# Kernel tuning notes

Measured on AMD Instinct MI355X. Metric: run time of the kernel, lower is better.

Reference implementation:

```python
import jax, jax.numpy as jnp
import numpy as np

B, S, IN = 64, 2048, 256          # batch, num_steps, input_size
MS, H, HD = 8, 8, 64              # mem_slots, num_heads, head_size
M = H * HD                        # mem_size = 512
KS = HD                           # key_size defaults to head_size
NG = 2 * M                        # num_gates (gate_style='unit')
TOPK = 3
EPS = 1e-5


def layernorm(x, g, b):
    mu = jnp.mean(x, axis=-1, keepdims=True)
    var = jnp.var(x, axis=-1, keepdims=True)
    return (x - mu) / jnp.sqrt(var + EPS) * g + b


def setup_inputs() -> dict:
    key = jax.random.key(0)
    ks = jax.random.split(key, 16)
    def w(k, shape, scale=0.02):
        return jax.random.normal(k, shape, dtype=jnp.float32) * scale
    return {
        "inputs": jax.random.normal(ks[0], (B, S, IN), dtype=jnp.float32),
        "memory": jax.random.normal(ks[1], (B, MS, M), dtype=jnp.float32),
        "Wq": w(ks[2], (M, H * KS)), "bq": jnp.zeros((H * KS,), jnp.float32),
        "Wk": w(ks[3], (M, H * KS)), "bk": jnp.zeros((H * KS,), jnp.float32),
        "Wv": w(ks[4], (M, H * HD)), "bv": jnp.zeros((H * HD,), jnp.float32),
        "Wmlp": w(ks[5], (M, M)), "bmlp": jnp.zeros((M,), jnp.float32),  # shared across both mlp layers ([Linear]*L)
        "g1": jnp.ones((M,), jnp.float32), "b1": jnp.zeros((M,), jnp.float32),
        "g2": jnp.ones((M,), jnp.float32), "b2": jnp.zeros((M,), jnp.float32),
        "Wi": w(ks[6], (IN, M)), "bi": jnp.zeros((M,), jnp.float32),  # input_projector
        "rw": jax.random.normal(ks[7], (M,), dtype=jnp.float32),       # RepeatLinear.w
        "Wr": w(ks[8], (M, NG)), "br": jnp.zeros((NG,), jnp.float32),  # RepeatLinear.linear
        "Wg": w(ks[9], (MS, M, NG)),                                   # GroupLinearLayer (no bias)
        "forget_bias": jnp.array(1.0, jnp.float32),
        "input_bias": jnp.array(0.0, jnp.float32),
    }


def reference(inputs, memory, Wq, bq, Wk, bk, Wv, bv, Wmlp, bmlp,
              g1, b1, g2, b2, Wi, bi, rw, Wr, br, Wg,
              forget_bias, input_bias):
    # input_projector (treat_input_as_matrix=True path)
    x = inputs @ Wi + bi                                   # [B,S,M]

    # --- multihead attention over memory (num_blocks=1) ---
    q = (memory @ Wq + bq).reshape(B, MS, H, KS).transpose(0, 2, 1, 3)   # [B,H,MS,KS]
    k = (x @ Wk + bk).reshape(B, S, H, KS).transpose(0, 2, 1, 3)         # [B,H,S,KS]
    v = (x @ Wv + bv).reshape(B, S, H, HD).transpose(0, 2, 1, 3)         # [B,H,S,HD]
    scores = jax.nn.softmax(jnp.einsum('bhmd,bhsd->bhms', q, k), axis=-1)  # no 1/sqrt(d) scale, per source
    # top-k mask over key/step axis, scatter of top-k indices -> multiplicative 0/1 mask
    _, idx = jax.lax.top_k(scores, TOPK)                   # [B,H,MS,TOPK]
    mask = jnp.sum(jax.nn.one_hot(idx, S, dtype=scores.dtype), axis=-2)  # [B,H,MS,S]
    scores = scores * mask
    att = jnp.einsum('bhms,bhsd->bhmd', scores, v)         # [B,H,MS,HD]
    att = att.transpose(0, 2, 1, 3).reshape(B, MS, M)      # [B,MS,M]

    mem1 = layernorm(memory + att, g1, b1)
    mlp = jax.nn.relu(mem1 @ Wmlp + bmlp)                  # attention_mlp layer (weights shared)
    mlp = jax.nn.relu(mlp @ Wmlp + bmlp)
    next_mem = layernorm(mem1 + mlp, g2, b2)

    # --- gates (computed from pre-attention memory, per forward_step) ---
    gate_in = jax.nn.relu(rw * x).mean(axis=1) @ Wr + br   # RepeatLinear -> [B,NG]
    gate_mem = jnp.einsum('bsd,sdo->bso', jnp.tanh(memory), Wg)  # GroupLinear -> [B,MS,NG]
    gates = gate_mem + gate_in[:, None, :]
    input_gate, forget_gate = jnp.split(gates, 2, axis=2)  # each [B,MS,M]
    input_gate = jax.nn.sigmoid(input_gate + input_bias)
    forget_gate = jax.nn.sigmoid(forget_gate + forget_bias)

    next_mem = input_gate * jnp.tanh(next_mem) + forget_gate * memory
    return next_mem.reshape(B, MS * M)
```

## Files before the change

### kernel.cpp

```cpp
#include <hip/hip_runtime.h>
#include <hip/hip_bf16.h>
#include <math.h>

#define BB 64
#define SS 2048
#define IN_ 256
#define MSLOT 8
#define HH 8
#define HD_ 64
#define MM 512
#define NG_ 1024

typedef __attribute__((ext_vector_type(8))) short short8;
typedef __attribute__((ext_vector_type(8))) unsigned short ushort8;
typedef __attribute__((ext_vector_type(4))) unsigned short ushort4v;
typedef __attribute__((ext_vector_type(4))) float f32x4;
typedef __attribute__((ext_vector_type(16))) float f32x16;
typedef unsigned long long u64;
typedef unsigned int u32;

__device__ __forceinline__ unsigned short f2bf(float f) {
    unsigned int u = __builtin_bit_cast(unsigned int, f);
    u += 0x7fff + ((u >> 16) & 1);
    return (unsigned short)(u >> 16);
}

__device__ __forceinline__ u64 score_key(float v, int idx) {
    u32 x = __float_as_uint(v);
    u32 fk = (x & 0x80000000u) ? ~x : (x | 0x80000000u);
    return ((u64)fk << 32) | (u32)(~(u32)idx);
}
__device__ __forceinline__ float key_val(u64 k) {
    u32 fk = (u32)(k >> 32);
    u32 x = (fk & 0x80000000u) ? (fk & 0x7FFFFFFFu) : ~fk;
    return __uint_as_float(x);
}
__device__ __forceinline__ int key_idx(u64 k) { return (int)(~(u32)k); }

__device__ __forceinline__ void merge3(u64& a0, u64& a1, u64& a2, u64 b0, u64 b1, u64 b2) {
    bool t0 = a0 >= b0;
    u64 m0 = t0 ? a0 : b0;
    u64 a0x = t0 ? a1 : a0, a1x = t0 ? a2 : a1;
    u64 b0x = t0 ? b0 : b1, b1x = t0 ? b1 : b2;
    bool t1 = a0x >= b0x;
    u64 m1 = t1 ? a0x : b0x;
    u64 a0y = t1 ? a1x : a0x;
    u64 b0y = t1 ? b0x : b1x;
    bool t2 = a0y >= b0y;
    u64 m2 = t2 ? a0y : b0y;
    a0 = m0; a1 = m1; a2 = m2;
}

__device__ __forceinline__ void merge3_shfl(u64& k0, u64& k1, u64& k2, int off) {
    u64 b0 = __shfl_xor(k0, off);
    u64 b1 = __shfl_xor(k1, off);
    u64 b2 = __shfl_xor(k2, off);
    merge3(k0, k1, k2, b0, b1, b2);
}

__device__ __forceinline__ float block_sum256(float v, float* red) {
    int t = threadIdx.x;
    red[t] = v; __syncthreads();
    for (int s = 128; s > 0; s >>= 1) {
        if (t < s) red[t] += red[t + s];
        __syncthreads();
    }
    float r = red[0];
    __syncthreads();
    return r;
}

__device__ __forceinline__ void stage_tile_f32cvt(unsigned short* lds,
                                                  const float* __restrict__ src,
                                                  int t) {
#pragma unroll
    for (int it = 0; it < 8; ++it) {
        int c = t + it * 256;
        int r = c >> 5, ch = c & 31;
        const float* p = src + (size_t)r * 256 + ch * 8;
        float4 f0 = *(const float4*)p;
        float4 f1 = *(const float4*)(p + 4);
        ushort8 v;
        v[0] = f2bf(f0.x); v[1] = f2bf(f0.y); v[2] = f2bf(f0.z); v[3] = f2bf(f0.w);
        v[4] = f2bf(f1.x); v[5] = f2bf(f1.y); v[6] = f2bf(f1.z); v[7] = f2bf(f1.w);
        int sch = ch ^ (r & 15);
        *(ushort8*)(lds + r * 256 + sch * 8) = v;
    }
}

__device__ __forceinline__ short8 frag_ld(const unsigned short* lds, int row, int chunk) {
    int sch = chunk ^ (row & 15);
    return *(const short8*)(lds + row * 256 + sch * 8);
}

__device__ __forceinline__ short8 frag_ld512(const unsigned short* lds, int row, int chunk) {
    int sch = chunk ^ (row & 7);
    return *(const short8*)(lds + row * 512 + sch * 8);
}

__global__ __launch_bounds__(256) void k_fuse_w(const float* __restrict__ Wi,
                                                const float* __restrict__ Wk,
                                                const float* __restrict__ Wv,
                                                const float* __restrict__ bi,
                                                const float* __restrict__ bv,
                                                float* __restrict__ WikT,
                                                float* __restrict__ Wiv,
                                                float* __restrict__ bvf) {
    int blk = blockIdx.x;
    int which = blk >> 9;
    int o = blk & 511;
    const float* W = which ? Wv : Wk;

    __shared__ float col[512];
    __shared__ float red[256];
    int t = threadIdx.x;
    col[t]       = W[t * 512 + o];
    col[t + 256] = W[(t + 256) * 512 + o];
    __syncthreads();

    const float* wi_row = Wi + t * 512;
    float acc = 0.f;
    for (int j = 0; j < 512; ++j) acc += wi_row[j] * col[j];
    if (which) Wiv[t * 512 + o] = acc;
    else       WikT[o * 256 + t] = acc;

    if (which) {
        float p = bi[t] * col[t] + bi[t + 256] * col[t + 256];
        float s = block_sum256(p, red);
        if (t == 0) bvf[o] = s + bv[o];
    }
}

__global__ __launch_bounds__(256) void k_q(const float* __restrict__ memory,
                                           const float* __restrict__ Wq,
                                           const float* __restrict__ bq,
                                           float* __restrict__ q) {
    int bms = blockIdx.x;
    __shared__ float row[512];
    int t = threadIdx.x;
    row[t]       = memory[bms * 512 + t];
    row[t + 256] = memory[bms * 512 + t + 256];
    __syncthreads();
    for (int oo = 0; oo < 2; ++oo) {
        int o = oo * 256 + t;
        float acc = bq[o];
        for (int j = 0; j < 512; ++j) acc += row[j] * Wq[j * 512 + o];
        q[bms * 512 + o] = acc;
    }
}

__global__ __launch_bounds__(256) void k_p(const float* __restrict__ q,
                                           const float* __restrict__ WikT,
                                           unsigned short* __restrict__ Pb) {
    int blk = blockIdx.x;
    int b = blk >> 6, hm = blk & 63;
    int h = hm >> 3, ms = hm & 7;
    int t = threadIdx.x;
    __shared__ float qv[64];
    if (t < 64) qv[t] = q[(b * 8 + ms) * 512 + h * 64 + t];
    __syncthreads();
    float acc = 0.f;
    for (int d = 0; d < 64; ++d) acc += qv[d] * WikT[(h * 64 + d) * 256 + t];
    Pb[blk * 256 + t] = f2bf(acc);
}

__global__ __launch_bounds__(256) void k_prep(const float* __restrict__ Wi,
                                              unsigned short* __restrict__ WiTf,
                                              const float* __restrict__ mem,
                                              unsigned short* __restrict__ tm,
                                              const float* __restrict__ Wmlp,
                                              unsigned short* __restrict__ WmlpTb) {
    int blk = blockIdx.x;
    int t = threadIdx.x;
    if (blk < 512) {
        int idx = blk * 256 + t;
        int e = idx & 7, l = (idx >> 3) & 63, ks = (idx >> 9) & 15, dtg = idx >> 13;
        int d = dtg * 32 + (l & 31);
        int k = ks * 16 + (l >> 5) * 8 + e;
        WiTf[idx] = f2bf(Wi[k * 512 + d]);
    } else if (blk < 768) {
        int i = ((blk - 512) * 256 + t) * 4;
        float4 v = *(const float4*)(mem + i);
        ushort4v o;
        o[0] = f2bf(tanhf(v.x)); o[1] = f2bf(tanhf(v.y));
        o[2] = f2bf(tanhf(v.z)); o[3] = f2bf(tanhf(v.w));
        *(ushort4v*)(tm + i) = o;
    } else {
        int o = blk - 768;
#pragma unroll
        for (int kk = 0; kk < 2; ++kk) {
            int k = kk * 256 + t;
            WmlpTb[o * 512 + k] = f2bf(Wmlp[k * 512 + o]);
        }
    }
}

__global__ __launch_bounds__(256) void k_big(const float* __restrict__ inputs,
                                             const unsigned short* __restrict__ Pb,
                                             const unsigned short* __restrict__ WiTf,
                                             const float* __restrict__ bi,
                                             const float* __restrict__ rw,
                                             uint4* __restrict__ statA,
                                             uint4* __restrict__ statB,
                                             float* __restrict__ giaccp) {
    __shared__ unsigned short Il[64 * 256];
    int t = threadIdx.x;
    int hw = blockIdx.x;
    int L = (hw & 7) * 256 + (hw >> 3);
    int b = L >> 5, stile = L & 31;
    int l = t & 63, w = t >> 6;
    int kg = l >> 4, r16 = l & 15;
    int l31 = l & 31, hi = l >> 5;

    stage_tile_f32cvt(Il, inputs + ((size_t)b * SS + stile * 64) * IN_, t);
    __syncthreads();

    f32x4 acc[4];
#pragma unroll
    for (int nt = 0; nt < 4; ++nt) acc[nt] = (f32x4){0.f, 0.f, 0.f, 0.f};
    {
        const unsigned short* pbase = Pb + ((size_t)(b * 64 + w * 16 + r16)) * 256;
#pragma unroll
        for (int kk = 0; kk < 8; ++kk) {
            short8 a = *(const short8*)(pbase + kk * 32 + kg * 8);
#pragma unroll
            for (int nt = 0; nt < 4; ++nt) {
                short8 bfr = frag_ld(Il, nt * 16 + r16, kk * 4 + kg);
                acc[nt] = __builtin_amdgcn_mfma_f32_16x16x32_bf16(a, bfr, acc[nt], 0, 0, 0);
            }
        }
    }

    int sbase = stile * 64;
#pragma unroll
    for (int j = 0; j < 4; ++j) {
        u64 k0 = 0, k1 = 0, k2 = 0;
#pragma unroll
        for (int nt = 0; nt < 4; ++nt) {
            u64 key = score_key(acc[nt][j], sbase + nt * 16 + r16);
            bool g0 = key > k0, g1 = key > k1, g2 = key > k2;
            k2 = g1 ? k1 : (g2 ? key : k2);
            k1 = g0 ? k0 : (g1 ? key : k1);
            k0 = g0 ? key : k0;
        }
        merge3_shfl(k0, k1, k2, 1);
        merge3_shfl(k0, k1, k2, 2);
        merge3_shfl(k0, k1, k2, 4);
        merge3_shfl(k0, k1, k2, 8);

        float m = key_val(k0);
        float se = 0.f;
#pragma unroll
        for (int nt = 0; nt < 4; ++nt) se += expf(acc[nt][j] - m);
#pragma unroll
        for (int off = 1; off <= 8; off <<= 1) se += __shfl_xor(se, off);

        if (r16 == 0) {
            int row = w * 16 + kg * 4 + j;
            int grow = (b * 64 + row) * 32 + stile;
            statA[grow] = make_uint4(__float_as_uint(se), (u32)(k0 >> 32), (u32)k0, (u32)(k1 >> 32));
            statB[grow] = make_uint4((u32)k1, (u32)(k2 >> 32), (u32)k2, 0u);
        }
    }

#pragma unroll 1
    for (int i = 0; i < 4; ++i) {
        int dtg = w * 4 + i;
        int d = dtg * 32 + l31;
        float bid = bi[d], rwd = rw[d];
        f32x16 g0 = {0.f,0.f,0.f,0.f,0.f,0.f,0.f,0.f,0.f,0.f,0.f,0.f,0.f,0.f,0.f,0.f};
        f32x16 g1 = {0.f,0.f,0.f,0.f,0.f,0.f,0.f,0.f,0.f,0.f,0.f,0.f,0.f,0.f,0.f,0.f};
#pragma unroll
        for (int ksh = 0; ksh < 2; ++ksh) {
            short8 wf[8];
#pragma unroll
            for (int ks8 = 0; ks8 < 8; ++ks8)
                wf[ks8] = *(const short8*)(WiTf + ((size_t)((dtg * 16 + ksh * 8 + ks8) * 64) + l) * 8);
#pragma unroll
            for (int ks8 = 0; ks8 < 8; ++ks8) {
                int ch = (ksh * 8 + ks8) * 2 + hi;
                short8 a0 = frag_ld(Il, l31, ch);
                g0 = __builtin_amdgcn_mfma_f32_32x32x16_bf16(a0, wf[ks8], g0, 0, 0, 0);
                short8 a1 = frag_ld(Il, 32 + l31, ch);
                g1 = __builtin_amdgcn_mfma_f32_32x32x16_bf16(a1, wf[ks8], g1, 0, 0, 0);
            }
        }
        float rs = 0.f;
#pragma unroll
        for (int jj = 0; jj < 16; ++jj) {
            rs += fmaxf(rwd * (g0[jj] + bid), 0.f);
            rs += fmaxf(rwd * (g1[jj] + bid), 0.f);
        }
        rs += __shfl_xor(rs, 32);
        if (hi == 0)
            giaccp[((size_t)stile * 64 + b) * 512 + d] = rs;
    }
}

__global__ __launch_bounds__(256) void k_combine(const uint4* __restrict__ statA,
                                                 const uint4* __restrict__ statB,
                                                 float* __restrict__ topk_p,
                                                 int* __restrict__ topk_idx) {
    int t = threadIdx.x;
    int row = blockIdx.x * 4 + (t >> 6);
    int l = t & 63;

    float s_c = 0.f, m_c = 0.f;
    u64 k0 = 0, k1 = 0, k2 = 0;
    if (l < 32) {
        uint4 A = statA[row * 32 + l];
        uint4 Bv = statB[row * 32 + l];
        s_c = __uint_as_float(A.x);
        k0 = ((u64)A.y << 32) | A.z;
        k1 = ((u64)A.w << 32) | Bv.x;
        k2 = ((u64)Bv.y << 32) | Bv.z;
        m_c = key_val(k0);
    }
    merge3_shfl(k0, k1, k2, 1);
    merge3_shfl(k0, k1, k2, 2);
    merge3_shfl(k0, k1, k2, 4);
    merge3_shfl(k0, k1, k2, 8);
    merge3_shfl(k0, k1, k2, 16);

    float M = key_val(k0);
    float S = (l < 32) ? s_c * expf(m_c - M) : 0.f;
#pragma unroll
    for (int off = 1; off <= 16; off <<= 1) S += __shfl_xor(S, off);

    if (l == 0) {
        u64 ks[3] = {k0, k1, k2};
#pragma unroll
        for (int r = 0; r < 3; ++r) {
            topk_p[row * 3 + r] = expf(key_val(ks[r]) - M) / S;
            topk_idx[row * 3 + r] = key_idx(ks[r]);
        }
    }
}

__global__ __launch_bounds__(256) void k_att2(const float* __restrict__ inputs,
                                              const float* __restrict__ Wiv,
                                              const float* __restrict__ bvf,
                                              const float* __restrict__ topk_p,
                                              const int* __restrict__ topk_idx,
                                              const float* __restrict__ memory,
                                              const float* __restrict__ g1,
                                              const float* __restrict__ b1,
                                              float* __restrict__ mem1) {
    int bms = blockIdx.x;
    int b = bms >> 3, ms = bms & 7;
    int t = threadIdx.x;
    __shared__ float w[8 * 256];
    __shared__ float ps[8];
    __shared__ float red[256];

#pragma unroll
    for (int h = 0; h < 8; ++h) {
        int row = (b * 64 + h * 8 + ms) * 3;
        float acc = 0.f, psum = 0.f;
#pragma unroll
        for (int j = 0; j < 3; ++j) {
            int sj = topk_idx[row + j];
            float pj = topk_p[row + j];
            acc += pj * inputs[((size_t)b * SS + sj) * IN_ + t];
            psum += pj;
        }
        w[h * 256 + t] = acc;
        if (t == 0) ps[h] = psum;
    }
    __syncthreads();

    float a_val[2];
#pragma unroll
    for (int oo = 0; oo < 2; ++oo) {
        int o = oo * 256 + t;
        int h = o >> 6;
        float acc = ps[h] * bvf[o];
        const float* wh = w + h * 256;
#pragma unroll 8
        for (int i = 0; i < 256; ++i) acc += wh[i] * Wiv[i * 512 + o];
        a_val[oo] = acc;
    }

    float m0 = memory[bms * 512 + t], m1 = memory[bms * 512 + t + 256];
    float x0 = m0 + a_val[0], x1 = m1 + a_val[1];
    float mu = block_sum256(x0 + x1, red) * (1.f / 512.f);
    float d0 = x0 - mu, d1 = x1 - mu;
    float var = block_sum256(d0 * d0 + d1 * d1, red) * (1.f / 512.f);
    float rstd = rsqrtf(var + 1e-5f);
    mem1[bms * 512 + t]       = d0 * rstd * g1[t] + b1[t];
    mem1[bms * 512 + t + 256] = d1 * rstd * g1[t + 256] + b1[t + 256];
}

__global__ __launch_bounds__(256) void k_gatein2(const float* __restrict__ giaccp,
                                                 const float* __restrict__ Wr,
                                                 const float* __restrict__ br,
                                                 float* __restrict__ gate_in) {
    int b = blockIdx.x >> 2, ot = blockIdx.x & 3;
    int t = threadIdx.x;
    int o = ot * 256 + t;
    __shared__ float gm[512];
    float s0 = 0.f, s1 = 0.f;
    for (int st = 0; st < 32; ++st) {
        s0 += giaccp[((size_t)st * 64 + b) * 512 + t];
        s1 += giaccp[((size_t)st * 64 + b) * 512 + t + 256];
    }
    gm[t]       = s0 * (1.0f / 2048.0f);
    gm[t + 256] = s1 * (1.0f / 2048.0f);
    __syncthreads();
    float acc = br[o];
#pragma unroll 8
    for (int d = 0; d < 512; ++d) acc += gm[d] * Wr[d * 1024 + o];
    gate_in[b * 1024 + o] = acc;
}

__global__ __launch_bounds__(256) void k_gates_mfma(const unsigned short* __restrict__ tmem_b,
                                                    const float* __restrict__ Wg,
                                                    const float* __restrict__ gate_in,
                                                    const float* __restrict__ fb,
                                                    const float* __restrict__ ib,
                                                    float* __restrict__ sg) {
    int ms = blockIdx.x >> 5;
    int otile = blockIdx.x & 31;
    int t = threadIdx.x;
    int l = t & 63, w = t >> 6;
    int kg = l >> 4, r16 = l & 15;
    __shared__ unsigned short Al[64 * 128];
    __shared__ unsigned short Bl[32 * 136];
    f32x4 acc[2];
#pragma unroll
    for (int nt = 0; nt < 2; ++nt) acc[nt] = (f32x4){0.f, 0.f, 0.f, 0.f};

    int o_l = t & 31;
    for (int kc = 0; kc < 4; ++kc) {
        __syncthreads();
#pragma unroll
        for (int it = 0; it < 4; ++it) {
            int c = t + it * 256;
            int r = c >> 4, ch = c & 15;
            ushort8 v = *(const ushort8*)(tmem_b + (size_t)(r * 8 + ms) * 512 + kc * 128 + ch * 8);
            int sch = ch ^ (r & 7);
            *(ushort8*)(Al + r * 128 + sch * 8) = v;
        }
#pragma unroll
        for (int i = 0; i < 16; ++i) {
            int k_l = (t >> 5) + 8 * i;
            float v = Wg[((size_t)ms * 512 + kc * 128 + k_l) * 1024 + otile * 32 + o_l];
            Bl[o_l * 136 + k_l] = f2bf(v);
        }
        __syncthreads();
#pragma unroll
        for (int kk = 0; kk < 4; ++kk) {
            int ch = kk * 4 + kg;
            short8 a = *(const short8*)(Al + (w * 16 + r16) * 128 + ((ch ^ (r16 & 7)) * 8));
#pragma unroll
            for (int nt = 0; nt < 2; ++nt) {
                short8 bfr = *(const short8*)(Bl + (nt * 16 + r16) * 136 + ch * 8);
                acc[nt] = __builtin_amdgcn_mfma_f32_16x16x32_bf16(a, bfr, acc[nt], 0, 0, 0);
            }
        }
    }
    float ibv = ib[0], fbv = fb[0];
#pragma unroll
    for (int nt = 0; nt < 2; ++nt) {
        int o = otile * 32 + nt * 16 + r16;
        float bias = (o < 512) ? ibv : fbv;
#pragma unroll
        for (int j = 0; j < 4; ++j) {
            int b = w * 16 + kg * 4 + j;
            float g = acc[nt][j] + gate_in[b * 1024 + o] + bias;
            sg[(size_t)(b * 8 + ms) * 1024 + o] = 1.f / (1.f + expf(-g));
        }
    }
}

__global__ __launch_bounds__(256) void k_mlp_mfma(const float* __restrict__ mem1,
                                                  const unsigned short* __restrict__ WmlpTb,
                                                  const float* __restrict__ bmlp,
                                                  const float* __restrict__ g2,
                                                  const float* __restrict__ b2,
                                                  const float* __restrict__ sg,
                                                  const float* __restrict__ memory,
                                                  float* __restrict__ out) {
    __shared__ unsigned short At[16 * 512];
    __shared__ unsigned short Bt[16 * 512];
    __shared__ float redS[64], redQ[64], muL[16], rsL[16];
    int blk = blockIdx.x;
    int rowbase = blk * 16;
    int t = threadIdx.x;
    int l = t & 63, w = t >> 6;
    int kg = l >> 4, r16 = l & 15;

#pragma unroll
    for (int it = 0; it < 4; ++it) {
        int c = t + it * 256;
        int r = c >> 6, ch = c & 63;
        const float* p = mem1 + (size_t)(rowbase + r) * 512 + ch * 8;
        float4 f0 = *(const float4*)p;
        float4 f1 = *(const float4*)(p + 4);
        ushort8 v;
        v[0] = f2bf(f0.x); v[1] = f2bf(f0.y); v[2] = f2bf(f0.z); v[3] = f2bf(f0.w);
        v[4] = f2bf(f1.x); v[5] = f2bf(f1.y); v[6] = f2bf(f1.z); v[7] = f2bf(f1.w);
        int sch = ch ^ (r & 7);
        *(ushort8*)(At + r * 512 + sch * 8) = v;
    }
    __syncthreads();

    f32x4 acc[8];
#pragma unroll
    for (int f = 0; f < 8; ++f) acc[f] = (f32x4){0.f, 0.f, 0.f, 0.f};
    for (int kk2 = 0; kk2 < 16; ++kk2) {
        short8 a = frag_ld512(At, r16, kk2 * 4 + kg);
#pragma unroll
        for (int f = 0; f < 8; ++f) {
            short8 bfr = *(const short8*)(WmlpTb + (size_t)(w * 128 + f * 16 + r16) * 512 + kk2 * 32 + kg * 8);
            acc[f] = __builtin_amdgcn_mfma_f32_16x16x32_bf16(a, bfr, acc[f], 0, 0, 0);
        }
    }
#pragma unroll
    for (int f = 0; f < 8; ++f) {
        int o = w * 128 + f * 16 + r16;
        float bm = bmlp[o];
        int ch = o >> 3, oe = o & 7;
#pragma unroll
        for (int j = 0; j < 4; ++j) {
            int row = kg * 4 + j;
            float v = fmaxf(acc[f][j] + bm, 0.f);
            Bt[row * 512 + ((ch ^ (row & 7)) * 8 + oe)] = f2bf(v);
        }
    }
    __syncthreads();

#pragma unroll
    for (int f = 0; f < 8; ++f) acc[f] = (f32x4){0.f, 0.f, 0.f, 0.f};
    for (int kk2 = 0; kk2 < 16; ++kk2) {
        short8 a = frag_ld512(Bt, r16, kk2 * 4 + kg);
#pragma unroll
        for (int f = 0; f < 8; ++f) {
            short8 bfr = *(const short8*)(WmlpTb + (size_t)(w * 128 + f * 16 + r16) * 512 + kk2 * 32 + kg * 8);
            acc[f] = __builtin_amdgcn_mfma_f32_16x16x32_bf16(a, bfr, acc[f], 0, 0, 0);
        }
    }

    float y[8][4];
    float ps[4] = {0.f, 0.f, 0.f, 0.f}, pq[4] = {0.f, 0.f, 0.f, 0.f};
#pragma unroll
    for (int f = 0; f < 8; ++f) {
        int o = w * 128 + f * 16 + r16;
        float bm = bmlp[o];
#pragma unroll
        for (int j = 0; j < 4; ++j) {
            int row = kg * 4 + j;
            float m1v = mem1[(size_t)(rowbase + row) * 512 + o];
            float v = m1v + fmaxf(acc[f][j] + bm, 0.f);
            y[f][j] = v;
            ps[j] += v;
            pq[j] += v * v;
        }
    }
#pragma unroll
    for (int j = 0; j < 4; ++j) {
#pragma unroll
        for (int off = 1; off <= 8; off <<= 1) {
            ps[j] += __shfl_xor(ps[j], off);
            pq[j] += __shfl_xor(pq[j], off);
        }
    }
    if (r16 == 0) {
#pragma unroll
        for (int j = 0; j < 4; ++j) {
            int row = kg * 4 + j;
            redS[row * 4 + w] = ps[j];
            redQ[row * 4 + w] = pq[j];
        }
    }
    __syncthreads();
    if (t < 16) {
        float s = redS[t * 4] + redS[t * 4 + 1] + redS[t * 4 + 2] + redS[t * 4 + 3];
        float q = redQ[t * 4] + redQ[t * 4 + 1] + redQ[t * 4 + 2] + redQ[t * 4 + 3];
        float mu = s * (1.f / 512.f);
        float var = q * (1.f / 512.f) - mu * mu;
        muL[t] = mu;
        rsL[t] = rsqrtf(var + 1e-5f);
    }
    __syncthreads();

#pragma unroll
    for (int f = 0; f < 8; ++f) {
        int o = w * 128 + f * 16 + r16;
        float g2v = g2[o], b2v = b2[o];
#pragma unroll
        for (int j = 0; j < 4; ++j) {
            int row = kg * 4 + j;
            int grow = rowbase + row;
            float np = (y[f][j] - muL[row]) * rsL[row] * g2v + b2v;
            float ig = sg[(size_t)grow * 1024 + o];
            float fg = sg[(size_t)grow * 1024 + 512 + o];
            float mv = memory[(size_t)grow * 512 + o];
            out[(size_t)grow * 512 + o] = ig * tanhf(np) + fg * mv;
        }
    }
}

extern "C" void kernel_launch(void* const* d_in, const int* in_sizes, int n_in,
                              void* d_out, int out_size, void* d_ws, size_t ws_size,
                              hipStream_t stream) {
    const float* inputs = (const float*)d_in[0];
    const float* memory = (const float*)d_in[1];
    const float* Wq  = (const float*)d_in[2];
    const float* bq  = (const float*)d_in[3];
    const float* Wk  = (const float*)d_in[4];
    const float* Wv  = (const float*)d_in[6];
    const float* bv  = (const float*)d_in[7];
    const float* Wmlp= (const float*)d_in[8];
    const float* bmlp= (const float*)d_in[9];
    const float* g1  = (const float*)d_in[10];
    const float* b1  = (const float*)d_in[11];
    const float* g2  = (const float*)d_in[12];
    const float* b2  = (const float*)d_in[13];
    const float* Wi  = (const float*)d_in[14];
    const float* bi  = (const float*)d_in[15];
    const float* rw  = (const float*)d_in[16];
    const float* Wr  = (const float*)d_in[17];
    const float* br  = (const float*)d_in[18];
    const float* Wg  = (const float*)d_in[19];
    const float* fb  = (const float*)d_in[20];
    const float* ib  = (const float*)d_in[21];
    float* out = (float*)d_out;

    float* ws = (float*)d_ws;
    float* WikT   = ws + 0;
    float* Wiv    = ws + 131072;
    float* bvf    = ws + 262144;
    float* qbuf   = ws + 263168;
    unsigned short* Pb   = (unsigned short*)(ws + 525312);
    unsigned short* WiTf = (unsigned short*)(ws + 1049600);
    uint4* statA  = (uint4*)(ws + 1115136);
    uint4* statB  = (uint4*)(ws + 1639424);
    float* topkp  = ws + 2163712;
    int*   topki  = (int*)(ws + 2176000);
    float* giaccp = ws + 2188288;
    float* gatein = ws + 3236864;
    float* sgbuf  = ws + 3302400;
    float* mem1   = ws + 3826688;
    unsigned short* tmem_b = (unsigned short*)(ws + 4088832);
    unsigned short* WmlpTb = (unsigned short*)(ws + 4219904);

    (void)in_sizes; (void)n_in; (void)out_size; (void)ws_size;

    k_fuse_w<<<1024, 256, 0, stream>>>(Wi, Wk, Wv, bi, bv, WikT, Wiv, bvf);
    k_q<<<512, 256, 0, stream>>>(memory, Wq, bq, qbuf);
    k_p<<<4096, 256, 0, stream>>>(qbuf, WikT, Pb);
    k_prep<<<1280, 256, 0, stream>>>(Wi, WiTf, memory, tmem_b, Wmlp, WmlpTb);
    k_big<<<2048, 256, 0, stream>>>(inputs, Pb, WiTf, bi, rw, statA, statB, giaccp);
    k_combine<<<1024, 256, 0, stream>>>(statA, statB, topkp, topki);
    k_gatein2<<<256, 256, 0, stream>>>(giaccp, Wr, br, gatein);
    k_gates_mfma<<<256, 256, 0, stream>>>(tmem_b, Wg, gatein, fb, ib, sgbuf);
    k_att2<<<512, 256, 0, stream>>>(inputs, Wiv, bvf, topkp, topki, memory, g1, b1, mem1);
    k_mlp_mfma<<<32, 256, 0, stream>>>(mem1, WmlpTb, bmlp, g2, b2, sgbuf, memory, out);
}
```

Before: 301.4 us.

## Tile weight-fusion and Q GEMMs, pack bf16 converts, restructure top-k via LDS

Replaces the per-column dot-product kernels for fusing Wi with Wk/Wv and for computing q with LDS-tiled 32x32 SGEMM kernels. Each thread now produces a 2x2 output block, which reuses weights and cuts redundant global reads. Float-to-bf16 conversion uses the packed v_cvt_pk_bf16_f32 instruction. The big scores kernel prefetches its P fragments into registers before staging the input tile. It then moves the per-row top-3 and softmax-sum work to an LDS transpose, where four threads cover each row with fewer shuffles. The trade-off is extra LDS traffic and syncs in the scores kernel, plus more registers for the prefetched fragments.

```diff
diff --git a/kernel.cpp b/kernel.cpp
--- a/kernel.cpp
+++ b/kernel.cpp
@@ -23,6 +23,12 @@
     unsigned int u = __builtin_bit_cast(unsigned int, f);
     u += 0x7fff + ((u >> 16) & 1);
     return (unsigned short)(u >> 16);
+}
+
+__device__ __forceinline__ u32 f2bf_pk(float a, float b) {
+    u32 r;
+    asm("v_cvt_pk_bf16_f32 %0, %1, %2" : "=v"(r) : "v"(a), "v"(b));
+    return r;
 }
 
 __device__ __forceinline__ u64 score_key(float v, int idx) {
@@ -80,11 +86,13 @@
         const float* p = src + (size_t)r * 256 + ch * 8;
         float4 f0 = *(const float4*)p;
         float4 f1 = *(const float4*)(p + 4);
-        ushort8 v;
-        v[0] = f2bf(f0.x); v[1] = f2bf(f0.y); v[2] = f2bf(f0.z); v[3] = f2bf(f0.w);
-        v[4] = f2bf(f1.x); v[5] = f2bf(f1.y); v[6] = f2bf(f1.z); v[7] = f2bf(f1.w);
+        uint4 v;
+        v.x = f2bf_pk(f0.x, f0.y);
+        v.y = f2bf_pk(f0.z, f0.w);
+        v.z = f2bf_pk(f1.x, f1.y);
+        v.w = f2bf_pk(f1.z, f1.w);
         int sch = ch ^ (r & 15);
-        *(ushort8*)(lds + r * 256 + sch * 8) = v;
+        *(uint4*)(lds + r * 256 + sch * 8) = v;
     }
 }
 
@@ -98,55 +106,109 @@
     return *(const short8*)(lds + row * 512 + sch * 8);
 }
 
-__global__ __launch_bounds__(256) void k_fuse_w(const float* __restrict__ Wi,
-                                                const float* __restrict__ Wk,
-                                                const float* __restrict__ Wv,
-                                                const float* __restrict__ bi,
-                                                const float* __restrict__ bv,
-                                                float* __restrict__ WikT,
-                                                float* __restrict__ Wiv,
-                                                float* __restrict__ bvf) {
+__global__ __launch_bounds__(256) void k_fuse_w2(const float* __restrict__ Wi,
+                                                 const float* __restrict__ Wk,
+                                                 const float* __restrict__ Wv,
+                                                 const float* __restrict__ bi,
+                                                 const float* __restrict__ bv,
+                                                 float* __restrict__ WikT,
+                                                 float* __restrict__ Wiv,
+                                                 float* __restrict__ bvf) {
     int blk = blockIdx.x;
-    int which = blk >> 9;
-    int o = blk & 511;
+    int t = threadIdx.x;
+    if (blk >= 256) {
+        int o = (blk - 256) * 256 + t;
+        float acc = bv[o];
+        for (int j = 0; j < 512; ++j) acc += bi[j] * Wv[j * 512 + o];
+        bvf[o] = acc;
+        return;
+    }
+    int which = blk >> 7;
+    int rem = blk & 127;
+    int ot = rem >> 3, it = rem & 7;
+    int o0 = ot * 32, i0 = it * 32;
     const float* W = which ? Wv : Wk;
 
-    __shared__ float col[512];
-    __shared__ float red[256];
-    int t = threadIdx.x;
-    col[t]       = W[t * 512 + o];
-    col[t + 256] = W[(t + 256) * 512 + o];
-    __syncthreads();
-
-    const float* wi_row = Wi + t * 512;
-    float acc = 0.f;
-    for (int j = 0; j < 512; ++j) acc += wi_row[j] * col[j];
-    if (which) Wiv[t * 512 + o] = acc;
-    else       WikT[o * 256 + t] = acc;
-
-    if (which) {
-        float p = bi[t] * col[t] + bi[t + 256] * col[t + 256];
-        float s = block_sum256(p, red);
-        if (t == 0) bvf[o] = s + bv[o];
-    }
-}
-
-__global__ __launch_bounds__(256) void k_q(const float* __restrict__ memory,
-                                           const float* __restrict__ Wq,
-                                           const float* __restrict__ bq,
-                                           float* __restrict__ q) {
-    int bms = blockIdx.x;
-    __shared__ float row[512];
-    int t = threadIdx.x;
-    row[t]       = memory[bms * 512 + t];
-    row[t + 256] = memory[bms * 512 + t + 256];
-    __syncthreads();
-    for (int oo = 0; oo < 2; ++oo) {
-        int o = oo * 256 + t;
-        float acc = bq[o];
-        for (int j = 0; j < 512; ++j) acc += row[j] * Wq[j * 512 + o];
-        q[bms * 512 + o] = acc;
-    }
+    __shared__ float As[64 * 33];
+    __shared__ float Bs[32 * 65];
+    int tx = t & 15, ty = t >> 4;
+
+    float acc[2][2] = {{0.f, 0.f}, {0.f, 0.f}};
+    for (int jc = 0; jc < 512; jc += 64) {
+        __syncthreads();
+#pragma unroll
+        for (int k = 0; k < 8; ++k) {
+            int idx = t + k * 256;
+            int jl = idx >> 5, ol = idx & 31;
+            As[jl * 33 + ol] = W[(jc + jl) * 512 + o0 + ol];
+        }
+#pragma unroll
+        for (int k = 0; k < 8; ++k) {
+            int idx = t + k * 256;
+            int il = idx >> 6, jl = idx & 63;
+            Bs[il * 65 + jl] = Wi[(i0 + il) * 512 + jc + jl];
+        }
+        __syncthreads();
+#pragma unroll 4
+        for (int jl = 0; jl < 64; ++jl) {
+            float a0 = As[jl * 33 + ty], a1 = As[jl * 33 + ty + 16];
+            float b0 = Bs[tx * 65 + jl], b1 = Bs[(tx + 16) * 65 + jl];
+            acc[0][0] += a0 * b0; acc[0][1] += a0 * b1;
+            acc[1][0] += a1 * b0; acc[1][1] += a1 * b1;
+        }
+    }
+#pragma unroll
+    for (int m = 0; m < 2; ++m)
+#pragma unroll
+        for (int n = 0; n < 2; ++n) {
+            int o = o0 + ty + 16 * m, i = i0 + tx + 16 * n;
+            if (which) Wiv[i * 512 + o] = acc[m][n];
+            else       WikT[o * 256 + i] = acc[m][n];
+        }
+}
+
+__global__ __launch_bounds__(256) void k_q2(const float* __restrict__ memory,
+                                            const float* __restrict__ Wq,
+                                            const float* __restrict__ bq,
+                                            float* __restrict__ q) {
+    int blk = blockIdx.x;
+    int bt = blk >> 4, ot2 = blk & 15;
+    int b0 = bt * 32, o0 = ot2 * 32;
+    int t = threadIdx.x;
+    __shared__ float Am[32 * 65];
+    __shared__ float Bq[64 * 33];
+    int tx = t & 15, ty = t >> 4;
+    float acc[2][2] = {{0.f, 0.f}, {0.f, 0.f}};
+    for (int jc = 0; jc < 512; jc += 64) {
+        __syncthreads();
+#pragma unroll
+        for (int k = 0; k < 8; ++k) {
+            int idx = t + k * 256;
+            int bl = idx >> 6, jl = idx & 63;
+            Am[bl * 65 + jl] = memory[(b0 + bl) * 512 + jc + jl];
+        }
+#pragma unroll
+        for (int k = 0; k < 8; ++k) {
+            int idx = t + k * 256;
+            int jl = idx >> 5, ol = idx & 31;
+            Bq[jl * 33 + ol] = Wq[(jc + jl) * 512 + o0 + ol];
+        }
+        __syncthreads();
+#pragma unroll 4
+        for (int jl = 0; jl < 64; ++jl) {
+            float a0 = Am[ty * 65 + jl], a1 = Am[(ty + 16) * 65 + jl];
+            float b0v = Bq[jl * 33 + tx], b1v = Bq[jl * 33 + tx + 16];
+            acc[0][0] += a0 * b0v; acc[0][1] += a0 * b1v;
+            acc[1][0] += a1 * b0v; acc[1][1] += a1 * b1v;
+        }
+    }
+#pragma unroll
+    for (int m = 0; m < 2; ++m)
+#pragma unroll
+        for (int n = 0; n < 2; ++n) {
+            int bms = b0 + ty + 16 * m, o = o0 + tx + 16 * n;
+            q[bms * 512 + o] = acc[m][n] + bq[o];
+        }
 }
 
 __global__ __launch_bounds__(256) void k_p(const float* __restrict__ q,
@@ -212,54 +274,26 @@
     int kg = l >> 4, r16 = l & 15;
     int l31 = l & 31, hi = l >> 5;
 
-    stage_tile_f32cvt(Il, inputs + ((size_t)b * SS + stile * 64) * IN_, t);
-    __syncthreads();
-
-    f32x4 acc[4];
-#pragma unroll
-    for (int nt = 0; nt < 4; ++nt) acc[nt] = (f32x4){0.f, 0.f, 0.f, 0.f};
+    short8 a[8];
     {
         const unsigned short* pbase = Pb + ((size_t)(b * 64 + w * 16 + r16)) * 256;
 #pragma unroll
-        for (int kk = 0; kk < 8; ++kk) {
-            short8 a = *(const short8*)(pbase + kk * 32 + kg * 8);
-#pragma unroll
-            for (int nt = 0; nt < 4; ++nt) {
-                short8 bfr = frag_ld(Il, nt * 16 + r16, kk * 4 + kg);
-                acc[nt] = __builtin_amdgcn_mfma_f32_16x16x32_bf16(a, bfr, acc[nt], 0, 0, 0);
-            }
-        }
-    }
-
-    int sbase = stile * 64;
-#pragma unroll
-    for (int j = 0; j < 4; ++j) {
-        u64 k0 = 0, k1 = 0, k2 = 0;
+        for (int kk = 0; kk < 8; ++kk)
+            a[kk] = *(const short8*)(pbase + kk * 32 + kg * 8);
+    }
+
+    stage_tile_f32cvt(Il, inputs + ((size_t)b * SS + stile * 64) * IN_, t);
+    __syncthreads();
+
+    f32x4 acc[4];
+#pragma unroll
+    for (int nt = 0; nt < 4; ++nt) acc[nt] = (f32x4){0.f, 0.f, 0.f, 0.f};
+#pragma unroll
+    for (int kk = 0; kk < 8; ++kk) {
 #pragma unroll
         for (int nt = 0; nt < 4; ++nt) {
-            u64 key = score_key(acc[nt][j], sbase + nt * 16 + r16);
-            bool g0 = key > k0, g1 = key > k1, g2 = key > k2;
-            k2 = g1 ? k1 : (g2 ? key : k2);
-            k1 = g0 ? k0 : (g1 ? key : k1);
-            k0 = g0 ? key : k0;
-        }
-        merge3_shfl(k0, k1, k2, 1);
-        merge3_shfl(k0, k1, k2, 2);
-        merge3_shfl(k0, k1, k2, 4);
-        merge3_shfl(k0, k1, k2, 8);
-
-        float m = key_val(k0);
-        float se = 0.f;
-#pragma unroll
-        for (int nt = 0; nt < 4; ++nt) se += expf(acc[nt][j] - m);
-#pragma unroll
-        for (int off = 1; off <= 8; off <<= 1) se += __shfl_xor(se, off);
-
-        if (r16 == 0) {
-            int row = w * 16 + kg * 4 + j;
-            int grow = (b * 64 + row) * 32 + stile;
-            statA[grow] = make_uint4(__float_as_uint(se), (u32)(k0 >> 32), (u32)k0, (u32)(k1 >> 32));
-            statB[grow] = make_uint4((u32)k1, (u32)(k2 >> 32), (u32)k2, 0u);
+            short8 bfr = frag_ld(Il, nt * 16 + r16, kk * 4 + kg);
+            acc[nt] = __builtin_amdgcn_mfma_f32_16x16x32_bf16(a[kk], bfr, acc[nt], 0, 0, 0);
         }
     }
 
@@ -294,6 +328,45 @@
         rs += __shfl_xor(rs, 32);
         if (hi == 0)
             giaccp[((size_t)stile * 64 + b) * 512 + d] = rs;
+    }
+
+    __syncthreads();
+    float* Sl = (float*)Il;
+#pragma unroll
+    for (int nt = 0; nt < 4; ++nt)
+#pragma unroll
+        for (int j = 0; j < 4; ++j)
+            Sl[(w * 16 + kg * 4 + j) * 65 + nt * 16 + r16] = acc[nt][j];
+    __syncthreads();
+
+    int row = t >> 2, cq = t & 3;
+    float v[16];
+#pragma unroll
+    for (int i = 0; i < 16; ++i) v[i] = Sl[row * 65 + cq * 16 + i];
+
+    u64 k0 = 0, k1 = 0, k2 = 0;
+#pragma unroll
+    for (int i = 0; i < 16; ++i) {
+        u64 key = score_key(v[i], stile * 64 + cq * 16 + i);
+        bool g0 = key > k0, g1 = key > k1, g2 = key > k2;
+        k2 = g1 ? k1 : (g2 ? key : k2);
+        k1 = g0 ? k0 : (g1 ? key : k1);
+        k0 = g0 ? key : k0;
+    }
+    merge3_shfl(k0, k1, k2, 1);
+    merge3_shfl(k0, k1, k2, 2);
+
+    float m = key_val(k0);
+    float se = 0.f;
+#pragma unroll
+    for (int i = 0; i < 16; ++i) se += expf(v[i] - m);
+    se += __shfl_xor(se, 1);
+    se += __shfl_xor(se, 2);
+
+    if (cq == 0) {
+        int grow = (b * 64 + row) * 32 + stile;
+        statA[grow] = make_uint4(__float_as_uint(se), (u32)(k0 >> 32), (u32)k0, (u32)(k1 >> 32));
+        statB[grow] = make_uint4((u32)k1, (u32)(k2 >> 32), (u32)k2, 0u);
     }
 }
 
@@ -497,11 +570,13 @@
         const float* p = mem1 + (size_t)(rowbase + r) * 512 + ch * 8;
         float4 f0 = *(const float4*)p;
         float4 f1 = *(const float4*)(p + 4);
-        ushort8 v;
-        v[0] = f2bf(f0.x); v[1] = f2bf(f0.y); v[2] = f2bf(f0.z); v[3] = f2bf(f0.w);
-        v[4] = f2bf(f1.x); v[5] = f2bf(f1.y); v[6] = f2bf(f1.z); v[7] = f2bf(f1.w);
+        uint4 v;
+        v.x = f2bf_pk(f0.x, f0.y);
+        v.y = f2bf_pk(f0.z, f0.w);
+        v.z = f2bf_pk(f1.x, f1.y);
+        v.w = f2bf_pk(f1.z, f1.w);
         int sch = ch ^ (r & 7);
-        *(ushort8*)(At + r * 512 + sch * 8) = v;
+        *(uint4*)(At + r * 512 + sch * 8) = v;
     }
     __syncthreads();
 
@@ -647,8 +722,8 @@
 
     (void)in_sizes; (void)n_in; (void)out_size; (void)ws_size;
 
-    k_fuse_w<<<1024, 256, 0, stream>>>(Wi, Wk, Wv, bi, bv, WikT, Wiv, bvf);
-    k_q<<<512, 256, 0, stream>>>(memory, Wq, bq, qbuf);
+    k_fuse_w2<<<258, 256, 0, stream>>>(Wi, Wk, Wv, bi, bv, WikT, Wiv, bvf);
+    k_q2<<<256, 256, 0, stream>>>(memory, Wq, bq, qbuf);
     k_p<<<4096, 256, 0, stream>>>(qbuf, WikT, Pb);
     k_prep<<<1280, 256, 0, stream>>>(Wi, WiTf, memory, tmem_b, Wmlp, WmlpTb);
     k_big<<<2048, 256, 0, stream>>>(inputs, Pb, WiTf, bi, rw, statA, statB, giaccp);
```

Result: no change. 300.5 us (-0.3%).
